# Performance work log

Measured on AMD Instinct MI355X. Metric: run time of the kernel, lower is better.

## Reference

```python
import jax, jax.numpy as jnp
import numpy as np

OCC_THR = 0.5
RADIUS = 1.0
BIG = 1e30  # stands in for float('inf') to stay autodiff/jit friendly


def setup_inputs() -> dict:
    key = jax.random.key(0)
    k1, k2 = jax.random.split(key)

    def cloud(k, n):
        kx, kp = jax.random.split(k)
        xyz = jax.random.uniform(kx, (n, 3), dtype=jnp.float32) * 20.0
        p = jax.random.uniform(kp, (n, 1), dtype=jnp.float32)
        return jnp.concatenate([xyz, p], axis=1)

    return {"pred_cloud": cloud(k1, 8192), "true_cloud": cloud(k2, 8192)}


def _spatial_prob_loss(pred_cloud, true_cloud):
    pred_xyz, pred_p = pred_cloud[:, :3], pred_cloud[:, 3]
    true_xyz, true_p = true_cloud[:, :3], true_cloud[:, 3]
    pred_occ = pred_p >= OCC_THR  # [Np]
    true_occ = true_p >= OCC_THR  # [Nt]

    # Pairwise distances [Nt, Np]; matching indices are non-differentiable
    # (same as torch: indices come out of argmin/.item()), so stop_gradient here.
    d = jnp.sqrt(jnp.sum((true_xyz[:, None, :] - pred_xyz[None, :, :]) ** 2, axis=-1))
    d = jax.lax.stop_gradient(d)
    # Invalidate: unoccupied true rows, unoccupied pred cols, and pairs beyond radius.
    valid = true_occ[:, None] & pred_occ[None, :] & (d <= RADIUS)
    d = jnp.where(valid, d, BIG)

    Np = pred_xyz.shape[0]

    # Greedy sequential matching: row-by-row argmin with column invalidation.
    def step(invalid_cols, row):
        r = jnp.where(invalid_cols, BIG, row)
        j = jnp.argmin(r)
        ok = r[j] < BIG
        invalid_cols = jnp.where(ok, invalid_cols.at[j].set(True), invalid_cols)
        return invalid_cols, (ok, j)

    _, (ok, match_j) = jax.lax.scan(step, jnp.zeros((Np,), dtype=bool), d)

    okf = ok.astype(pred_cloud.dtype)  # [Nt] 1.0 where true point i got matched
    n_matched = jnp.sum(okf)

    # Recompute matched distances differentiably via the (constant) indices.
    md = jnp.linalg.norm(true_xyz - pred_xyz[match_j], axis=-1)  # [Nt]
    mean_dist = jnp.sum(md * okf) / n_matched

    num_unmatched = jnp.sum(true_occ).astype(pred_cloud.dtype) - n_matched
    spatial_error = mean_dist + RADIUS * 10.0 * num_unmatched

    prob_mse = jnp.sum(((true_p - pred_p[match_j]) ** 2) * okf) / n_matched
    prob_error = prob_mse + num_unmatched
    return spatial_error + prob_error


def reference(pred_cloud, true_cloud):
    return _spatial_prob_loss(pred_cloud, true_cloud)
```

## Files before the change

kernel.cpp:

```cpp
#include <hip/hip_runtime.h>

#define NP      8192
#define NCG     20
#define NC3     8000
#define CELLCAP 8
#define NBLK    128
#define ROWS_PB 64
#define SEG_PB  160
#define ECAP    (NBLK*SEG_PB)
#define CAP     16
#define INF_U   0xFFFFFFFFu

__global__ __launch_bounds__(1024)
void build_cands(const float4* __restrict__ pred,
                 const float4* __restrict__ truec,
                 unsigned int* __restrict__ ocg,
                 unsigned short* __restrict__ Eg) {
    __shared__ unsigned short slot[NC3 * CELLCAP];
    __shared__ unsigned int cc[NC3 / 2];
    __shared__ unsigned long long skey[ROWS_PB][CAP];
    __shared__ int scnt[ROWS_PB];
    __shared__ int sst[ROWS_PB];
    int tid = threadIdx.x;
    int g = tid >> 4, l = tid & 15;

    for (int c = tid; c < NC3 / 2; c += 1024) cc[c] = 0;
    if (l == 0) scnt[g] = 0;
    __syncthreads();

    #pragma unroll
    for (int k = 0; k < 8; ++k) {
        int i = k * 1024 + tid;
        float4 p = pred[i];
        if (p.w >= 0.5f) {
            int cx = min((int)p.x, NCG - 1);
            int cy = min((int)p.y, NCG - 1);
            int cz = min((int)p.z, NCG - 1);
            int cell = (cz * NCG + cy) * NCG + cx;
            int sh = (cell & 1) * 16;
            unsigned int old = atomicAdd(&cc[cell >> 1], 1u << sh);
            int rk = (int)((old >> sh) & 0xFFFFu);
            if (rk < CELLCAP) slot[cell * CELLCAP + rk] = (unsigned short)i;
        }
    }
    __syncthreads();

    int row = blockIdx.x * ROWS_PB + g;
    float4 t = truec[row];
    if (t.w >= 0.5f) {
        int cx = min((int)t.x, NCG - 1);
        int cy = min((int)t.y, NCG - 1);
        int cz = min((int)t.z, NCG - 1);
        for (int ci = l; ci < 27; ci += 16) {
            int zz = cz + ci / 9 - 1;
            int yy = cy + (ci / 3) % 3 - 1;
            int xx = cx + ci % 3 - 1;
            if (zz < 0 || zz >= NCG || yy < 0 || yy >= NCG || xx < 0 || xx >= NCG)
                continue;
            int cell = (zz * NCG + yy) * NCG + xx;
            int cnt = (int)((cc[cell >> 1] >> ((cell & 1) * 16)) & 0xFFFFu);
            if (cnt > CELLCAP) cnt = CELLCAP;
            int sbase = cell * CELLCAP;
            for (int k = 0; k < cnt; ++k) {
                int j = slot[sbase + k];
                float4 pp = pred[j];
                float dx = t.x - pp.x, dy = t.y - pp.y, dz = t.z - pp.z;
                float d = sqrtf(dx * dx + dy * dy + dz * dz);
                if (d <= 1.0f) {
                    int a = atomicAdd(&scnt[g], 1);
                    if (a < CAP)
                        skey[g][a] = ((unsigned long long)__float_as_uint(d) << 32)
                                     | (unsigned int)j;
                }
            }
        }
    }
    __syncthreads();
    if (l == 0) {
        int n = min(scnt[g], CAP);
        for (int a = 1; a < n; ++a) {
            unsigned long long kv = skey[g][a];
            int b = a - 1;
            while (b >= 0 && skey[g][b] > kv) { skey[g][b + 1] = skey[g][b]; --b; }
            skey[g][b + 1] = kv;
        }
        scnt[g] = n;
    }
    __syncthreads();
    if (tid < ROWS_PB) {
        int n = scnt[tid];
        int inc = n;
        #pragma unroll
        for (int o = 1; o < 64; o <<= 1) {
            int u = __shfl_up(inc, o);
            if (tid >= o) inc += u;
        }
        int st = inc - n;
        int nn = n;
        if (st >= SEG_PB) nn = 0;
        else if (st + nn > SEG_PB) nn = SEG_PB - st;
        sst[tid] = st;
        scnt[tid] = nn;
        int r = blockIdx.x * ROWS_PB + tid;
        unsigned int occ2 = (truec[r].w >= 0.5f) ? 1u : 0u;
        unsigned int start = (nn > 0) ? (unsigned int)(blockIdx.x * SEG_PB + st) : 0u;
        ocg[r] = (occ2 << 31) | (start << 8) | (unsigned int)nn;
    }
    __syncthreads();
    {
        int st = blockIdx.x * SEG_PB + sst[g];
        int nn = scnt[g];
        for (int k = l; k < nn; k += 16)
            Eg[st + k] = (unsigned short)(skey[g][k] & 0x1FFFu);
    }
}

__global__ __launch_bounds__(1024)
void match_reduce(const float4* __restrict__ pred,
                  const float4* __restrict__ truec,
                  const unsigned int* __restrict__ ocg,
                  const unsigned short* __restrict__ Eg,
                  float* __restrict__ out) {
    __shared__ unsigned short E[ECAP];
    __shared__ unsigned int ocs[NP];
    __shared__ unsigned int Hs[NP];
    __shared__ float redf[2][16];
    __shared__ int redi[2][16];
    int tid = threadIdx.x;
    #pragma unroll
    for (int x = tid; x < ECAP / 8; x += 1024)
        ((uint4*)E)[x] = ((const uint4*)Eg)[x];
    #pragma unroll
    for (int x = tid; x < NP / 4; x += 1024)
        ((uint4*)ocs)[x] = ((const uint4*)ocg)[x];
    #pragma unroll
    for (int x = tid; x < NP / 4; x += 1024)
        ((uint4*)Hs)[x] = make_uint4(INF_U, INF_U, INF_U, INF_U);
    __syncthreads();

    int mynocc = 0;
    #pragma unroll
    for (int base = 0; base < NP; base += 2048) {
        int rA = base + tid, rB = base + 1024 + tid;
        unsigned int ocA = ocs[rA], ocB = ocs[rB];
        mynocc += (int)(ocA >> 31) + (int)(ocB >> 31);
        int nA = (int)(ocA & 0xFFu), nB = (int)(ocB & 0xFFu);
        int rAc = rA, rBc = rB;
        int pA = 0, pB = 0;
        int eA = (int)((ocA >> 8) & 0x7FFFFFu);
        int eB = (int)((ocB >> 8) & 0x7FFFFFu);
        bool aA = (nA > 0), aB = (nB > 0);
        while (aA || aB) {
            unsigned int colA = 0, colB = 0;
            if (aA) colA = E[eA];
            if (aB) colB = E[eB];
            unsigned int keyA = ((unsigned int)rAc << 4) | (unsigned int)pA;
            unsigned int keyB = ((unsigned int)rBc << 4) | (unsigned int)pB;
            unsigned int oldA = 0, oldB = 0;
            if (aA) oldA = atomicMin(&Hs[colA], keyA);
            if (aB) oldB = atomicMin(&Hs[colB], keyB);
            if (aA) {
                if (oldA > keyA) {
                    if (oldA == INF_U) aA = false;
                    else {
                        rAc = (int)(oldA >> 4);
                        pA = (int)(oldA & 15u) + 1;
                        unsigned int oc = ocs[rAc];
                        nA = (int)(oc & 0xFFu);
                        if (pA >= nA) aA = false;
                        else eA = (int)((oc >> 8) & 0x7FFFFFu) + pA;
                    }
                } else {
                    if (++pA >= nA) aA = false;
                    else ++eA;
                }
            }
            if (aB) {
                if (oldB > keyB) {
                    if (oldB == INF_U) aB = false;
                    else {
                        rBc = (int)(oldB >> 4);
                        pB = (int)(oldB & 15u) + 1;
                        unsigned int oc = ocs[rBc];
                        nB = (int)(oc & 0xFFu);
                        if (pB >= nB) aB = false;
                        else eB = (int)((oc >> 8) & 0x7FFFFFu) + pB;
                    }
                } else {
                    if (++pB >= nB) aB = false;
                    else ++eB;
                }
            }
        }
    }
    __syncthreads();

    float sdist = 0.f, sprob = 0.f;
    int nm = 0;
    for (int j = tid; j < NP; j += 1024) {
        unsigned int h = Hs[j];
        if (h != INF_U) {
            int r = (int)(h >> 4);
            float4 tt = truec[r];
            float4 pp = pred[j];
            float dx = tt.x - pp.x, dy = tt.y - pp.y, dz = tt.z - pp.z;
            sdist += sqrtf(dx * dx + dy * dy + dz * dz);
            float dp = tt.w - pp.w;
            sprob += dp * dp;
            ++nm;
        }
    }
    for (int o = 32; o; o >>= 1) {
        sdist += __shfl_down(sdist, o);
        sprob += __shfl_down(sprob, o);
        nm     += __shfl_down(nm, o);
        mynocc += __shfl_down(mynocc, o);
    }
    int wave = tid >> 6, lane = tid & 63;
    if (lane == 0) {
        redf[0][wave] = sdist; redf[1][wave] = sprob;
        redi[0][wave] = nm;    redi[1][wave] = mynocc;
    }
    __syncthreads();
    if (tid == 0) {
        float S = 0.f, P = 0.f; int NM = 0, NO = 0;
        for (int w = 0; w < 16; ++w) {
            S += redf[0][w]; P += redf[1][w];
            NM += redi[0][w]; NO += redi[1][w];
        }
        float nmf = (float)NM;
        float unm = (float)NO - nmf;
        out[0] = (S / nmf + 10.0f * unm) + (P / nmf + unm);
    }
}

extern "C" void kernel_launch(void* const* d_in, const int* in_sizes, int n_in,
                              void* d_out, int out_size, void* d_ws, size_t ws_size,
                              hipStream_t stream) {
    const float4* pred  = (const float4*)d_in[0];
    const float4* truec = (const float4*)d_in[1];
    float* out = (float*)d_out;

    unsigned int* ocg   = (unsigned int*)d_ws;
    unsigned short* Eg  = (unsigned short*)(ocg + NP);

    build_cands <<<NBLK, 1024, 0, stream>>>(pred, truec, ocg, Eg);
    match_reduce<<<1,    1024, 0, stream>>>(pred, truec, ocg, Eg, out);
}
```

Measured before the change: 28.78 us.

## Use four refillable matching lanes per thread and precompute candidate distances

The single-block matching loop now keeps four independent insertion chains per thread, pulling a new row from a work queue whenever a chain ends. Idle lanes get refilled rather than sitting out until both chains in a pair finish, and more atomicMin operations are in flight at once. The build kernel also stores each candidate's distance and squared probability difference in a workspace array, so the final reduction reads one float2 instead of two global float4 loads and a sqrt. This adds register pressure and an extra global write/read stream, and the workspace offset is hard-coded.

```diff
diff --git a/kernel.cpp b/kernel.cpp
--- a/kernel.cpp
+++ b/kernel.cpp
@@ -15,7 +15,8 @@
 void build_cands(const float4* __restrict__ pred,
                  const float4* __restrict__ truec,
                  unsigned int* __restrict__ ocg,
-                 unsigned short* __restrict__ Eg) {
+                 unsigned short* __restrict__ Eg,
+                 float2* __restrict__ cdp) {
     __shared__ unsigned short slot[NC3 * CELLCAP];
     __shared__ unsigned int cc[NC3 / 2];
     __shared__ unsigned long long skey[ROWS_PB][CAP];
@@ -110,16 +111,21 @@
     {
         int st = blockIdx.x * SEG_PB + sst[g];
         int nn = scnt[g];
-        for (int k = l; k < nn; k += 16)
-            Eg[st + k] = (unsigned short)(skey[g][k] & 0x1FFFu);
+        for (int k = l; k < nn; k += 16) {
+            unsigned long long kv = skey[g][k];
+            int j = (int)(kv & 0x1FFFu);
+            Eg[st + k] = (unsigned short)j;
+            float d = __uint_as_float((unsigned int)(kv >> 32));
+            float dp = t.w - pred[j].w;
+            cdp[st + k] = make_float2(d, dp * dp);
+        }
     }
 }
 
 __global__ __launch_bounds__(1024)
-void match_reduce(const float4* __restrict__ pred,
-                  const float4* __restrict__ truec,
-                  const unsigned int* __restrict__ ocg,
+void match_reduce(const unsigned int* __restrict__ ocg,
                   const unsigned short* __restrict__ Eg,
+                  const float2* __restrict__ cdp,
                   float* __restrict__ out) {
     __shared__ unsigned short E[ECAP];
     __shared__ unsigned int ocs[NP];
@@ -139,60 +145,61 @@
     __syncthreads();
 
     int mynocc = 0;
-    #pragma unroll
-    for (int base = 0; base < NP; base += 2048) {
-        int rA = base + tid, rB = base + 1024 + tid;
-        unsigned int ocA = ocs[rA], ocB = ocs[rB];
-        mynocc += (int)(ocA >> 31) + (int)(ocB >> 31);
-        int nA = (int)(ocA & 0xFFu), nB = (int)(ocB & 0xFFu);
-        int rAc = rA, rBc = rB;
-        int pA = 0, pB = 0;
-        int eA = (int)((ocA >> 8) & 0x7FFFFFu);
-        int eB = (int)((ocB >> 8) & 0x7FFFFFu);
-        bool aA = (nA > 0), aB = (nB > 0);
-        while (aA || aB) {
-            unsigned int colA = 0, colB = 0;
-            if (aA) colA = E[eA];
-            if (aB) colB = E[eB];
-            unsigned int keyA = ((unsigned int)rAc << 4) | (unsigned int)pA;
-            unsigned int keyB = ((unsigned int)rBc << 4) | (unsigned int)pB;
-            unsigned int oldA = 0, oldB = 0;
-            if (aA) oldA = atomicMin(&Hs[colA], keyA);
-            if (aB) oldB = atomicMin(&Hs[colB], keyB);
-            if (aA) {
-                if (oldA > keyA) {
-                    if (oldA == INF_U) aA = false;
-                    else {
-                        rAc = (int)(oldA >> 4);
-                        pA = (int)(oldA & 15u) + 1;
-                        unsigned int oc = ocs[rAc];
-                        nA = (int)(oc & 0xFFu);
-                        if (pA >= nA) aA = false;
-                        else eA = (int)((oc >> 8) & 0x7FFFFFu) + pA;
-                    }
-                } else {
-                    if (++pA >= nA) aA = false;
-                    else ++eA;
-                }
-            }
-            if (aB) {
-                if (oldB > keyB) {
-                    if (oldB == INF_U) aB = false;
-                    else {
-                        rBc = (int)(oldB >> 4);
-                        pB = (int)(oldB & 15u) + 1;
-                        unsigned int oc = ocs[rBc];
-                        nB = (int)(oc & 0xFFu);
-                        if (pB >= nB) aB = false;
-                        else eB = (int)((oc >> 8) & 0x7FFFFFu) + pB;
-                    }
-                } else {
-                    if (++pB >= nB) aB = false;
-                    else ++eB;
-                }
-            }
-        }
-    }
+    int nextk = 0;
+    bool a0 = false, a1 = false, a2 = false, a3 = false;
+    int r0 = 0, p0 = 0, n0 = 0, e0 = 0;
+    int r1 = 0, p1 = 0, n1 = 0, e1 = 0;
+    int r2 = 0, p2 = 0, n2 = 0, e2 = 0;
+    int r3 = 0, p3 = 0, n3 = 0, e3 = 0;
+
+#define REFILL(A, R, P, N, EE)                                          \
+    while (!A && nextk < 8) {                                           \
+        int row_ = nextk * 1024 + tid; ++nextk;                         \
+        unsigned int oc_ = ocs[row_];                                   \
+        mynocc += (int)(oc_ >> 31);                                     \
+        int nn_ = (int)(oc_ & 0xFFu);                                   \
+        if (nn_) { A = true; R = row_; P = 0; N = nn_;                  \
+                   EE = (int)((oc_ >> 8) & 0x7FFFFFu); }                \
+    }
+#define RESOLVE(A, R, P, N, EE, OLD)                                    \
+    if (A) {                                                            \
+        unsigned int key_ = ((unsigned int)R << 4) | (unsigned int)P;   \
+        if (OLD > key_) {                                               \
+            if (OLD == INF_U) A = false;                                \
+            else {                                                      \
+                R = (int)(OLD >> 4); P = (int)(OLD & 15u) + 1;          \
+                unsigned int oc_ = ocs[R];                              \
+                N = (int)(oc_ & 0xFFu);                                 \
+                if (P >= N) A = false;                                  \
+                else EE = (int)((oc_ >> 8) & 0x7FFFFFu) + P;            \
+            }                                                           \
+        } else {                                                        \
+            if (++P >= N) A = false; else ++EE;                         \
+        }                                                               \
+    }
+
+    REFILL(a0, r0, p0, n0, e0)
+    REFILL(a1, r1, p1, n1, e1)
+    REFILL(a2, r2, p2, n2, e2)
+    REFILL(a3, r3, p3, n3, e3)
+    while (a0 || a1 || a2 || a3) {
+        unsigned int c0 = 0, c1 = 0, c2 = 0, c3 = 0;
+        if (a0) c0 = E[e0];
+        if (a1) c1 = E[e1];
+        if (a2) c2 = E[e2];
+        if (a3) c3 = E[e3];
+        unsigned int o0 = 0, o1 = 0, o2 = 0, o3 = 0;
+        if (a0) o0 = atomicMin(&Hs[c0], ((unsigned int)r0 << 4) | (unsigned int)p0);
+        if (a1) o1 = atomicMin(&Hs[c1], ((unsigned int)r1 << 4) | (unsigned int)p1);
+        if (a2) o2 = atomicMin(&Hs[c2], ((unsigned int)r2 << 4) | (unsigned int)p2);
+        if (a3) o3 = atomicMin(&Hs[c3], ((unsigned int)r3 << 4) | (unsigned int)p3);
+        RESOLVE(a0, r0, p0, n0, e0, o0) REFILL(a0, r0, p0, n0, e0)
+        RESOLVE(a1, r1, p1, n1, e1, o1) REFILL(a1, r1, p1, n1, e1)
+        RESOLVE(a2, r2, p2, n2, e2, o2) REFILL(a2, r2, p2, n2, e2)
+        RESOLVE(a3, r3, p3, n3, e3, o3) REFILL(a3, r3, p3, n3, e3)
+    }
+#undef REFILL
+#undef RESOLVE
     __syncthreads();
 
     float sdist = 0.f, sprob = 0.f;
@@ -201,12 +208,12 @@
         unsigned int h = Hs[j];
         if (h != INF_U) {
             int r = (int)(h >> 4);
-            float4 tt = truec[r];
-            float4 pp = pred[j];
-            float dx = tt.x - pp.x, dy = tt.y - pp.y, dz = tt.z - pp.z;
-            sdist += sqrtf(dx * dx + dy * dy + dz * dz);
-            float dp = tt.w - pp.w;
-            sprob += dp * dp;
+            int p = (int)(h & 15u);
+            unsigned int oc = ocs[r];
+            int e = (int)((oc >> 8) & 0x7FFFFFu) + p;
+            float2 v = cdp[e];
+            sdist += v.x;
+            sprob += v.y;
             ++nm;
         }
     }
@@ -243,7 +250,8 @@
 
     unsigned int* ocg   = (unsigned int*)d_ws;
     unsigned short* Eg  = (unsigned short*)(ocg + NP);
-
-    build_cands <<<NBLK, 1024, 0, stream>>>(pred, truec, ocg, Eg);
-    match_reduce<<<1,    1024, 0, stream>>>(pred, truec, ocg, Eg, out);
+    float2* cdp         = (float2*)((char*)d_ws + 73728);
+
+    build_cands <<<NBLK, 1024, 0, stream>>>(pred, truec, ocg, Eg, cdp);
+    match_reduce<<<1,    1024, 0, stream>>>(ocg, Eg, cdp, out);
 }
```

Measured after the change: 33.15 us. 15.2% more time.
